# Kernel tuning notes

Measured on AMD Instinct MI355X. Metric: run time of the kernel, lower is better.

## Reference

```python
import jax, jax.numpy as jnp
import numpy as np

NUM_GRAPHS = 64


def gcn_conv(x, W, b, src, dst, deg_inv_sqrt, n_nodes):
    # x: [N, Fin] -> [N, Fout]; src/dst include self-loops
    h = x @ W                                   # [N, Fout]
    norm = deg_inv_sqrt[src] * deg_inv_sqrt[dst]  # [E+N]
    msg = h[src] * norm[:, None]                # gather + scale
    out = jax.ops.segment_sum(msg, dst, num_segments=n_nodes)  # scatter-add
    return out + b


def setup_inputs() -> dict:
    key = jax.random.key(0)
    ks = jax.random.split(key, 12)
    N, E, IND, H, OUT = 100000, 1600000, 128, 64, 2
    x = jax.random.normal(ks[0], (N, IND), dtype=jnp.float32)
    edge_index = jax.random.randint(ks[1], (2, E), 0, N, dtype=jnp.int64)
    batch = jnp.sort(jax.random.randint(ks[2], (N,), 0, NUM_GRAPHS, dtype=jnp.int64))
    def glorot(k, shape):
        lim = (6.0 / (shape[0] + shape[1])) ** 0.5
        return jax.random.uniform(k, shape, jnp.float32, -lim, lim)
    W1 = glorot(ks[3], (IND, 84)); b1 = jnp.zeros((84,), jnp.float32)
    W2 = glorot(ks[4], (84, H));   b2 = jnp.zeros((H,), jnp.float32)
    W3 = glorot(ks[5], (H, 32));   b3 = jnp.zeros((32,), jnp.float32)
    Wl = glorot(ks[6], (32, OUT)); bl = jnp.zeros((OUT,), jnp.float32)
    return {"x": x, "edge_index": edge_index, "batch": batch,
            "W1": W1, "b1": b1, "W2": W2, "b2": b2,
            "W3": W3, "b3": b3, "Wl": Wl, "bl": bl}


def reference(x, edge_index, batch, W1, b1, W2, b2, W3, b3, Wl, bl):
    n = x.shape[0]
    loops = jnp.arange(n, dtype=edge_index.dtype)
    # GCNConv adds self-loops before symmetric normalization
    src = jnp.concatenate([edge_index[0], loops])
    dst = jnp.concatenate([edge_index[1], loops])
    deg = jax.ops.segment_sum(jnp.ones_like(dst, dtype=x.dtype), dst, num_segments=n)
    dis = jnp.where(deg > 0, jax.lax.rsqrt(jnp.maximum(deg, 1.0)), 0.0)

    h = jax.nn.relu(gcn_conv(x, W1, b1, src, dst, dis, n))
    h = jax.nn.relu(gcn_conv(h, W2, b2, src, dst, dis, n))
    h = jax.nn.relu(gcn_conv(h, W3, b3, src, dst, dis, n))

    # global mean pool over graphs
    sums = jax.ops.segment_sum(h, batch, num_segments=NUM_GRAPHS)      # [G, 32]
    cnts = jax.ops.segment_sum(jnp.ones((n,), h.dtype), batch, num_segments=NUM_GRAPHS)
    pooled = sums / jnp.maximum(cnts, 1.0)[:, None]
    # dropout is identity in eval mode
    return pooled @ Wl + bl
```

## Files before the change

### kernel.cpp

```cpp
#include <hip/hip_runtime.h>
#include <hip/hip_bf16.h>

typedef __attribute__((ext_vector_type(8))) short bf16x8;
typedef __attribute__((ext_vector_type(4))) float f32x4;

__device__ inline short f2bf(float f) {
    __hip_bfloat16 h = __float2bfloat16(f);
    return *reinterpret_cast<short*>(&h);
}


__global__ void zero_k(float* __restrict__ p, int n) {
    for (int i = blockIdx.x * blockDim.x + threadIdx.x; i < n;
         i += gridDim.x * blockDim.x)
        p[i] = 0.0f;
}


__global__ __launch_bounds__(256) void bucket_hist_k(
    const int* __restrict__ dst, int* __restrict__ T, int E, int NB)
{
    __shared__ int hist[512];
    for (int b = threadIdx.x; b < NB; b += 256) hist[b] = 0;
    __syncthreads();
    int per = (E + gridDim.x - 1) / gridDim.x;
    int s = blockIdx.x * per;
    int e = min(E, s + per);
    for (int i = s + threadIdx.x; i < e; i += 256)
        atomicAdd(&hist[dst[i] >> 8], 1);
    __syncthreads();
    for (int b = threadIdx.x; b < NB; b += 256)
        T[b * gridDim.x + blockIdx.x] = hist[b];
}

__global__ __launch_bounds__(256) void scan_block_k(
    const int* __restrict__ in, int* __restrict__ out,
    int* __restrict__ bsum, int n)
{
    __shared__ int ts[256];
    int base = blockIdx.x * 2048;
    int i0 = base + threadIdx.x * 8;
    int vals[8];
    int s = 0;
#pragma unroll
    for (int j = 0; j < 8; ++j) {
        int v = (i0 + j) < n ? in[i0 + j] : 0;
        vals[j] = v; s += v;
    }
    ts[threadIdx.x] = s;
    __syncthreads();
    for (int d = 1; d < 256; d <<= 1) {
        int t = (threadIdx.x >= (unsigned)d) ? ts[threadIdx.x - d] : 0;
        __syncthreads();
        ts[threadIdx.x] += t;
        __syncthreads();
    }
    int run = ts[threadIdx.x] - s;
    if (threadIdx.x == 255) bsum[blockIdx.x] = ts[255];
#pragma unroll
    for (int j = 0; j < 8; ++j) {
        if (i0 + j < n) out[i0 + j] = run;
        run += vals[j];
    }
}

__global__ void scan_partials_k(int* __restrict__ bsum, int nb) {
    if (threadIdx.x == 0 && blockIdx.x == 0) {
        int run = 0;
        for (int i = 0; i < nb; ++i) { int t = bsum[i]; bsum[i] = run; run += t; }
    }
}

__global__ void scan_add_k(int* __restrict__ rp, const int* __restrict__ bsum,
                           int n, int E)
{
    int i = blockIdx.x * blockDim.x + threadIdx.x;
    if (i < n) rp[i] += bsum[i >> 11];
    if (i == 0) rp[n] = E;
}

__global__ __launch_bounds__(256) void bucket_scatter_k(
    const int* __restrict__ src, const int* __restrict__ dst,
    const int* __restrict__ Tsc, unsigned* __restrict__ pairs, int E, int NB)
{
    __shared__ int cur[512];
    for (int b = threadIdx.x; b < NB; b += 256)
        cur[b] = Tsc[b * gridDim.x + blockIdx.x];
    __syncthreads();
    int per = (E + gridDim.x - 1) / gridDim.x;
    int s = blockIdx.x * per;
    int e = min(E, s + per);
    for (int i = s + threadIdx.x; i < e; i += 256) {
        int d = dst[i];
        int pos = atomicAdd(&cur[d >> 8], 1);
        pairs[pos] = ((unsigned)(d & 255) << 24) | (unsigned)src[i];
    }
}

__global__ __launch_bounds__(256) void bucket_csr_k(
    const unsigned* __restrict__ pairs, const int* __restrict__ Tsc,
    int* __restrict__ row_ptr, float* __restrict__ dis,
    int* __restrict__ csr, int N, int E, int NB, int G)
{
    __shared__ int cnt[256];
    __shared__ int ts[256];
    __shared__ int cur[256];
    const int b = blockIdx.x;
    const int node0 = b << 8;
    const int e0 = Tsc[b * G];
    const int e1 = Tsc[(b + 1) * G];
    const int j = threadIdx.x;
    cnt[j] = 0;
    __syncthreads();
    for (int i = e0 + j; i < e1; i += 256)
        atomicAdd(&cnt[pairs[i] >> 24], 1);
    __syncthreads();
    int c = cnt[j];
    ts[j] = c;
    __syncthreads();
    for (int d = 1; d < 256; d <<= 1) {
        int t = (j >= d) ? ts[j - d] : 0;
        __syncthreads();
        ts[j] += t;
        __syncthreads();
    }
    int excl = ts[j] - c;
    int node = node0 + j;
    if (node < N) {
        row_ptr[node] = e0 + excl;
        dis[node] = rsqrtf(1.0f + (float)c);
    }
    cur[j] = e0 + excl;
    if (b == NB - 1 && j == 0) row_ptr[N] = E;
    __syncthreads();
    for (int i = e0 + j; i < e1; i += 256) {
        unsigned p = pairs[i];
        int pos = atomicAdd(&cur[p >> 24], 1);
        csr[pos] = (int)(p & 0xFFFFFFu);
    }
}


template<int FIN, int FOUT, int NKK, int CT>
__global__ void wfrag_build_k(const float* __restrict__ W,
                              __hip_bfloat16* __restrict__ out)
{
    int idx = blockIdx.x * 256 + threadIdx.x;
    if (idx >= CT * NKK * 64 * 8) return;
    int e = idx & 7;
    int lane = (idx >> 3) & 63;
    int t = idx >> 9;
    int kk = t % NKK, nn = t / NKK;
    int col = nn * 16 + (lane & 15);
    int k = kk * 32 + (lane >> 4) * 8 + e;
    float v = (k < FIN && col < FOUT) ? W[k * FOUT + col] : 0.f;
    out[idx] = __float2bfloat16(v);
}


template<int FIN>
__device__ inline bf16x8 load_a8f(const float* __restrict__ p, int k0) {
    bf16x8 r;
    if (k0 + 8 <= FIN) {
        float4 v0 = *reinterpret_cast<const float4*>(p + k0);
        float4 v1 = *reinterpret_cast<const float4*>(p + k0 + 4);
        r[0] = f2bf(v0.x); r[1] = f2bf(v0.y); r[2] = f2bf(v0.z); r[3] = f2bf(v0.w);
        r[4] = f2bf(v1.x); r[5] = f2bf(v1.y); r[6] = f2bf(v1.z); r[7] = f2bf(v1.w);
    } else {
#pragma unroll
        for (int e = 0; e < 8; ++e)
            r[e] = (k0 + e < FIN) ? f2bf(p[k0 + e]) : (short)0;
    }
    return r;
}

template<int FIN>
__device__ inline bf16x8 load_a8b(const __hip_bfloat16* __restrict__ p, int k0) {
    if (k0 + 8 <= FIN)
        return *reinterpret_cast<const bf16x8*>(p + k0);
    bf16x8 r;
    const short* ps = (const short*)p;
#pragma unroll
    for (int e = 0; e < 8; ++e)
        r[e] = (k0 + e < FIN) ? ps[k0 + e] : (short)0;
    return r;
}

template<typename TIN, int FIN, int SIN, int FOUT, int HS, int NKK, int CT>
__global__ __launch_bounds__(256) void gemm_mfma_v6(
    const TIN* __restrict__ in, const __hip_bfloat16* __restrict__ wfrag,
    const float* __restrict__ dis, __hip_bfloat16* __restrict__ hh, int n)
{
    const int tid = threadIdx.x;
    const long long base = (long long)blockIdx.x * 64;
    const int cnt = (int)min((long long)64, (long long)n - base);
    const int wv = tid >> 6, lane = tid & 63;
    const int rlo = lane & 15, kg = lane >> 4, kb = kg * 8;
    const int arow = wv * 16 + rlo;
    const long long row = base + arow;

    bf16x8 a[NKK];
    if (arow < cnt) {
        const TIN* p = &in[(size_t)row * SIN];
#pragma unroll
        for (int kk = 0; kk < NKK; ++kk) {
            if constexpr (sizeof(TIN) == 4)
                a[kk] = load_a8f<FIN>((const float*)p, kk * 32 + kb);
            else
                a[kk] = load_a8b<FIN>((const __hip_bfloat16*)p, kk * 32 + kb);
        }
    } else {
#pragma unroll
        for (int kk = 0; kk < NKK; ++kk)
            a[kk] = (bf16x8){0, 0, 0, 0, 0, 0, 0, 0};
    }

    f32x4 acc[CT];
#pragma unroll
    for (int nn = 0; nn < CT; ++nn) acc[nn] = (f32x4){0.f, 0.f, 0.f, 0.f};

#pragma unroll
    for (int nn = 0; nn < CT; ++nn) {
#pragma unroll
        for (int kk = 0; kk < NKK; ++kk) {
            bf16x8 b = *reinterpret_cast<const bf16x8*>(
                &wfrag[(size_t)((nn * NKK + kk) * 64 + lane) * 8]);
            acc[nn] = __builtin_amdgcn_mfma_f32_16x16x32_bf16(a[kk], b, acc[nn], 0, 0, 0);
        }
    }

    const int r0 = wv * 16 + kg * 4;
    float dv[4];
#pragma unroll
    for (int i = 0; i < 4; ++i)
        dv[i] = (r0 + i < cnt) ? dis[base + r0 + i] : 0.f;
#pragma unroll
    for (int nn = 0; nn < CT; ++nn) {
        const int col = nn * 16 + rlo;
        if (col < FOUT) {
#pragma unroll
            for (int i = 0; i < 4; ++i) {
                int r = r0 + i;
                if (r < cnt) {
                    __hip_bfloat16 o = __float2bfloat16(acc[nn][i] * dv[i]);
                    hh[(size_t)(base + r) * HS + col] = o;
                }
            }
        }
    }
}


template<int F, int HS, int SO, typename TOUT>
__global__ __launch_bounds__(256) void aggregate_v5(
    const __hip_bfloat16* __restrict__ hh, const int* __restrict__ row_ptr,
    const int* __restrict__ csr, const float* __restrict__ dis,
    const float* __restrict__ b, TOUT* __restrict__ out, int n)
{
    constexpr int FG = F / 4;
    long long idx = (long long)blockIdx.x * 256 + threadIdx.x;
    if (idx >= (long long)n * FG) return;
    int node = (int)(idx / FG);
    int fg = (int)(idx - (long long)node * FG);
    const int bf = fg * 4;

    const unsigned short* hs = (const unsigned short*)hh;
    auto lo16 = [](unsigned u) { return __uint_as_float(u << 16); };
    auto hi16 = [](unsigned u) { return __uint_as_float(u & 0xFFFF0000u); };

    uint2 su = *reinterpret_cast<const uint2*>(&hs[(size_t)node * HS + bf]);
    float a0 = lo16(su.x), a1 = hi16(su.x), a2 = lo16(su.y), a3 = hi16(su.y);
    float c0 = 0.f, c1 = 0.f, c2 = 0.f, c3 = 0.f;

    int e = row_ptr[node];
    const int e1 = row_ptr[node + 1];
    for (; e + 8 <= e1; e += 8) {
        int s0 = csr[e],     s1 = csr[e + 1], s2 = csr[e + 2], s3 = csr[e + 3];
        int s4 = csr[e + 4], s5 = csr[e + 5], s6 = csr[e + 6], s7 = csr[e + 7];
        uint2 u0 = *reinterpret_cast<const uint2*>(&hs[(size_t)s0 * HS + bf]);
        uint2 u1 = *reinterpret_cast<const uint2*>(&hs[(size_t)s1 * HS + bf]);
        uint2 u2 = *reinterpret_cast<const uint2*>(&hs[(size_t)s2 * HS + bf]);
        uint2 u3 = *reinterpret_cast<const uint2*>(&hs[(size_t)s3 * HS + bf]);
        uint2 u4 = *reinterpret_cast<const uint2*>(&hs[(size_t)s4 * HS + bf]);
        uint2 u5 = *reinterpret_cast<const uint2*>(&hs[(size_t)s5 * HS + bf]);
        uint2 u6 = *reinterpret_cast<const uint2*>(&hs[(size_t)s6 * HS + bf]);
        uint2 u7 = *reinterpret_cast<const uint2*>(&hs[(size_t)s7 * HS + bf]);
        a0 += lo16(u0.x); a1 += hi16(u0.x); a2 += lo16(u0.y); a3 += hi16(u0.y);
        c0 += lo16(u1.x); c1 += hi16(u1.x); c2 += lo16(u1.y); c3 += hi16(u1.y);
        a0 += lo16(u2.x); a1 += hi16(u2.x); a2 += lo16(u2.y); a3 += hi16(u2.y);
        c0 += lo16(u3.x); c1 += hi16(u3.x); c2 += lo16(u3.y); c3 += hi16(u3.y);
        a0 += lo16(u4.x); a1 += hi16(u4.x); a2 += lo16(u4.y); a3 += hi16(u4.y);
        c0 += lo16(u5.x); c1 += hi16(u5.x); c2 += lo16(u5.y); c3 += hi16(u5.y);
        a0 += lo16(u6.x); a1 += hi16(u6.x); a2 += lo16(u6.y); a3 += hi16(u6.y);
        c0 += lo16(u7.x); c1 += hi16(u7.x); c2 += lo16(u7.y); c3 += hi16(u7.y);
    }
    if (e + 4 <= e1) {
        int s0 = csr[e], s1 = csr[e + 1], s2 = csr[e + 2], s3 = csr[e + 3];
        uint2 u0 = *reinterpret_cast<const uint2*>(&hs[(size_t)s0 * HS + bf]);
        uint2 u1 = *reinterpret_cast<const uint2*>(&hs[(size_t)s1 * HS + bf]);
        uint2 u2 = *reinterpret_cast<const uint2*>(&hs[(size_t)s2 * HS + bf]);
        uint2 u3 = *reinterpret_cast<const uint2*>(&hs[(size_t)s3 * HS + bf]);
        a0 += lo16(u0.x); a1 += hi16(u0.x); a2 += lo16(u0.y); a3 += hi16(u0.y);
        c0 += lo16(u1.x); c1 += hi16(u1.x); c2 += lo16(u1.y); c3 += hi16(u1.y);
        a0 += lo16(u2.x); a1 += hi16(u2.x); a2 += lo16(u2.y); a3 += hi16(u2.y);
        c0 += lo16(u3.x); c1 += hi16(u3.x); c2 += lo16(u3.y); c3 += hi16(u3.y);
        e += 4;
    }
    for (; e < e1; ++e) {
        int s = csr[e];
        uint2 u = *reinterpret_cast<const uint2*>(&hs[(size_t)s * HS + bf]);
        a0 += lo16(u.x); a1 += hi16(u.x); a2 += lo16(u.y); a3 += hi16(u.y);
    }
    a0 += c0; a1 += c1; a2 += c2; a3 += c3;

    float d = dis[node];
    float4 bb = *reinterpret_cast<const float4*>(&b[bf]);
    float r0 = fmaxf(fmaf(d, a0, bb.x), 0.0f);
    float r1 = fmaxf(fmaf(d, a1, bb.y), 0.0f);
    float r2 = fmaxf(fmaf(d, a2, bb.z), 0.0f);
    float r3 = fmaxf(fmaf(d, a3, bb.w), 0.0f);

    if constexpr (sizeof(TOUT) == 2) {
        alignas(8) __hip_bfloat16 o[4];
        o[0] = __float2bfloat16(r0);
        o[1] = __float2bfloat16(r1);
        o[2] = __float2bfloat16(r2);
        o[3] = __float2bfloat16(r3);
        *reinterpret_cast<uint2*>(&((__hip_bfloat16*)out)[(size_t)node * SO + bf]) =
            *reinterpret_cast<const uint2*>(o);
    } else {
        float4 o;
        o.x = r0; o.y = r1; o.z = r2; o.w = r3;
        *reinterpret_cast<float4*>(&((float*)out)[(size_t)node * SO + bf]) = o;
    }
}


__global__ __launch_bounds__(256) void pool2_k(
    const float* __restrict__ h, const int* __restrict__ batch,
    float* __restrict__ sums, float* __restrict__ cnt, int n)
{
    constexpr int CHUNK = 1024;
    __shared__ float s[64 * 32];
    __shared__ float sc[64];
    for (int i = threadIdx.x; i < 64 * 32; i += 256) s[i] = 0.0f;
    if (threadIdx.x < 64) sc[threadIdx.x] = 0.0f;
    __syncthreads();

    long long start = (long long)blockIdx.x * CHUNK;
    long long end = start + CHUNK < n ? start + CHUNK : n;
    int total = (int)(end - start) * 32;
    for (int i = threadIdx.x; i < total; i += 256) {
        int r = i >> 5;
        int f = i & 31;
        int node = (int)start + r;
        int g = batch[node];
        atomicAdd(&s[g * 32 + f], h[(size_t)node * 32 + f]);
        if (f == 0) atomicAdd(&sc[g], 1.0f);
    }
    __syncthreads();
    for (int i = threadIdx.x; i < 64 * 32; i += 256) {
        float v = s[i];
        if (v != 0.0f) atomicAdd(&sums[i], v);
    }
    if (threadIdx.x < 64) {
        float v = sc[threadIdx.x];
        if (v != 0.0f) atomicAdd(&cnt[threadIdx.x], v);
    }
}

__global__ void head_k(const float* __restrict__ sums, const float* __restrict__ cnt,
                       const float* __restrict__ Wl, const float* __restrict__ bl,
                       float* __restrict__ out)
{
    int tid = threadIdx.x;
    if (tid < 128) {
        int g = tid >> 1;
        int o = tid & 1;
        float c = fmaxf(cnt[g], 1.0f);
        float a = 0.0f;
#pragma unroll
        for (int f = 0; f < 32; ++f)
            a += (sums[g * 32 + f] / c) * Wl[f * 2 + o];
        out[tid] = a + bl[o];
    }
}


extern "C" void kernel_launch(void* const* d_in, const int* in_sizes, int n_in,
                              void* d_out, int out_size, void* d_ws, size_t ws_size,
                              hipStream_t stream)
{
    const float* x   = (const float*)d_in[0];
    const int*   ei  = (const int*)d_in[1];
    const int*   bat = (const int*)d_in[2];
    const float* W1  = (const float*)d_in[3];
    const float* b1  = (const float*)d_in[4];
    const float* W2  = (const float*)d_in[5];
    const float* b2  = (const float*)d_in[6];
    const float* W3  = (const float*)d_in[7];
    const float* b3  = (const float*)d_in[8];
    const float* Wl  = (const float*)d_in[9];
    const float* bl  = (const float*)d_in[10];

    const int N = in_sizes[0] / 128;
    const int E = in_sizes[1] / 2;
    const int* src = ei;
    const int* dst = ei + E;

    const int NB = (N + 255) >> 8;
    const int G  = 128;
    const int NBG = NB * G;

    char* ws = (char*)d_ws;
    size_t off = 0;
    auto alloc = [&](size_t bytes) -> char* {
        char* p = ws + off;
        off += (bytes + 255) & ~(size_t)255;
        return p;
    };
    float* dis     = (float*)alloc((size_t)N * 4);
    int*   row_ptr = (int*)  alloc((size_t)(N + 1) * 4);
    int*   bsum    = (int*)  alloc(256 * 4);
    int*   csr     = (int*)  alloc((size_t)E * 4);
    int*   T       = (int*)  alloc((size_t)NBG * 4);
    int*   Tsc     = (int*)  alloc((size_t)(NBG + 1) * 4);
    __hip_bfloat16* WF1 = (__hip_bfloat16*)alloc(6 * 4 * 512 * 2);
    __hip_bfloat16* WF2 = (__hip_bfloat16*)alloc(4 * 3 * 512 * 2);
    __hip_bfloat16* WF3 = (__hip_bfloat16*)alloc(2 * 2 * 512 * 2);
    __hip_bfloat16* A = (__hip_bfloat16*)alloc((size_t)N * 96 * 2);
    __hip_bfloat16* B = (__hip_bfloat16*)alloc((size_t)N * 96 * 2);
    __hip_bfloat16* C = (__hip_bfloat16*)alloc((size_t)N * 64 * 2);
    float* D       = (float*)alloc((size_t)(64 * 32 + 64) * 4);
    unsigned* pairs = (unsigned*)C;

    dim3 blk(256);
    auto cdiv = [](long long a, long long b) { return (int)((a + b - 1) / b); };

    wfrag_build_k<128, 84, 4, 6><<<cdiv(6 * 4 * 512, 256), blk, 0, stream>>>(W1, WF1);
    wfrag_build_k< 84, 64, 3, 4><<<cdiv(4 * 3 * 512, 256), blk, 0, stream>>>(W2, WF2);
    wfrag_build_k< 64, 32, 2, 2><<<cdiv(2 * 2 * 512, 256), blk, 0, stream>>>(W3, WF3);

    bucket_hist_k<<<G, blk, 0, stream>>>(dst, T, E, NB);
    int nb_scan = cdiv(NBG, 2048);
    scan_block_k<<<nb_scan, blk, 0, stream>>>(T, Tsc, bsum, NBG);
    scan_partials_k<<<1, 64, 0, stream>>>(bsum, nb_scan);
    scan_add_k<<<cdiv(NBG, 256), blk, 0, stream>>>(Tsc, bsum, NBG, E);
    bucket_scatter_k<<<G, blk, 0, stream>>>(src, dst, Tsc, pairs, E, NB);
    bucket_csr_k<<<NB, blk, 0, stream>>>(pairs, Tsc, row_ptr, dis, csr, N, E, NB, G);

    gemm_mfma_v6<float, 128, 128, 84, 96, 4, 6><<<cdiv(N, 64), blk, 0, stream>>>(x, WF1, dis, A, N);
    aggregate_v5<84, 96, 96, __hip_bfloat16><<<cdiv((long long)N * 21, 256), blk, 0, stream>>>(
        A, row_ptr, csr, dis, b1, B, N);

    gemm_mfma_v6<__hip_bfloat16, 84, 96, 64, 64, 3, 4><<<cdiv(N, 64), blk, 0, stream>>>(B, WF2, dis, A, N);
    aggregate_v5<64, 64, 64, __hip_bfloat16><<<cdiv((long long)N * 16, 256), blk, 0, stream>>>(
        A, row_ptr, csr, dis, b2, C, N);

    gemm_mfma_v6<__hip_bfloat16, 64, 64, 32, 32, 2, 2><<<cdiv(N, 64), blk, 0, stream>>>(C, WF3, dis, A, N);
    aggregate_v5<32, 32, 32, float><<<cdiv((long long)N * 8, 256), blk, 0, stream>>>(
        A, row_ptr, csr, dis, b3, (float*)B, N);

    zero_k<<<cdiv(64 * 32 + 64, 256), blk, 0, stream>>>(D, 64 * 32 + 64);
    pool2_k<<<cdiv(N, 1024), blk, 0, stream>>>((float*)B, bat, D, D + 64 * 32, N);
    head_k<<<1, 128, 0, stream>>>(D, D + 64 * 32, Wl, bl, (float*)d_out);
}
```

Measured before the change: 288.8 us.

## Fuse final aggregation with mean pooling and merge weight-fragment kernels

The last GCN aggregation now pools directly: each thread aggregates its node's 4 features, applies bias and ReLU, and accumulates into shared-memory per-graph sums. This removes the fp32 intermediate write and read and one kernel launch. The three weight-fragment build kernels are merged into one launch, and the zeroing kernel is replaced by a memset. The cost is more shared-memory atomics per block, now spread across 256 node-features rather than chunked by 1024 nodes, and many more global atomic flushes because there are more blocks.

```diff
diff --git a/kernel.cpp b/kernel.cpp
--- a/kernel.cpp
+++ b/kernel.cpp
@@ -7,13 +7,6 @@
 __device__ inline short f2bf(float f) {
     __hip_bfloat16 h = __float2bfloat16(f);
     return *reinterpret_cast<short*>(&h);
-}
-
-
-__global__ void zero_k(float* __restrict__ p, int n) {
-    for (int i = blockIdx.x * blockDim.x + threadIdx.x; i < n;
-         i += gridDim.x * blockDim.x)
-        p[i] = 0.0f;
 }
 
 
@@ -141,12 +134,10 @@
 }
 
 
-template<int FIN, int FOUT, int NKK, int CT>
-__global__ void wfrag_build_k(const float* __restrict__ W,
-                              __hip_bfloat16* __restrict__ out)
-{
-    int idx = blockIdx.x * 256 + threadIdx.x;
-    if (idx >= CT * NKK * 64 * 8) return;
+__device__ inline void wfrag_seg(const float* __restrict__ W,
+                                 __hip_bfloat16* __restrict__ out, int idx,
+                                 int FIN, int FOUT, int NKK)
+{
     int e = idx & 7;
     int lane = (idx >> 3) & 63;
     int t = idx >> 9;
@@ -155,6 +146,17 @@
     int k = kk * 32 + (lane >> 4) * 8 + e;
     float v = (k < FIN && col < FOUT) ? W[k * FOUT + col] : 0.f;
     out[idx] = __float2bfloat16(v);
+}
+
+__global__ void wfrag_all_k(const float* __restrict__ W1,
+                            const float* __restrict__ W2,
+                            const float* __restrict__ W3,
+                            __hip_bfloat16* __restrict__ WF)
+{
+    int idx = blockIdx.x * 256 + threadIdx.x;
+    if (idx < 12288)       wfrag_seg(W1, WF,          idx,          128, 84, 4);
+    else if (idx < 18432)  wfrag_seg(W2, WF + 12288,  idx - 12288,   84, 64, 3);
+    else if (idx < 20480)  wfrag_seg(W3, WF + 18432,  idx - 18432,   64, 32, 2);
 }
 
 
@@ -336,27 +338,87 @@
 }
 
 
-__global__ __launch_bounds__(256) void pool2_k(
-    const float* __restrict__ h, const int* __restrict__ batch,
+__global__ __launch_bounds__(256) void agg_pool_k(
+    const __hip_bfloat16* __restrict__ hh, const int* __restrict__ row_ptr,
+    const int* __restrict__ csr, const float* __restrict__ dis,
+    const float* __restrict__ b, const int* __restrict__ batch,
     float* __restrict__ sums, float* __restrict__ cnt, int n)
 {
-    constexpr int CHUNK = 1024;
     __shared__ float s[64 * 32];
     __shared__ float sc[64];
     for (int i = threadIdx.x; i < 64 * 32; i += 256) s[i] = 0.0f;
     if (threadIdx.x < 64) sc[threadIdx.x] = 0.0f;
     __syncthreads();
 
-    long long start = (long long)blockIdx.x * CHUNK;
-    long long end = start + CHUNK < n ? start + CHUNK : n;
-    int total = (int)(end - start) * 32;
-    for (int i = threadIdx.x; i < total; i += 256) {
-        int r = i >> 5;
-        int f = i & 31;
-        int node = (int)start + r;
+    constexpr int HS = 32;
+    long long idx = (long long)blockIdx.x * 256 + threadIdx.x;
+    if (idx < (long long)n * 8) {
+        int node = (int)(idx >> 3);
+        int fg = (int)(idx & 7);
+        const int bf = fg * 4;
+
+        const unsigned short* hs = (const unsigned short*)hh;
+        auto lo16 = [](unsigned u) { return __uint_as_float(u << 16); };
+        auto hi16 = [](unsigned u) { return __uint_as_float(u & 0xFFFF0000u); };
+
+        uint2 su = *reinterpret_cast<const uint2*>(&hs[(size_t)node * HS + bf]);
+        float a0 = lo16(su.x), a1 = hi16(su.x), a2 = lo16(su.y), a3 = hi16(su.y);
+        float c0 = 0.f, c1 = 0.f, c2 = 0.f, c3 = 0.f;
+
+        int e = row_ptr[node];
+        const int e1 = row_ptr[node + 1];
+        for (; e + 8 <= e1; e += 8) {
+            int s0 = csr[e],     s1 = csr[e + 1], s2 = csr[e + 2], s3 = csr[e + 3];
+            int s4 = csr[e + 4], s5 = csr[e + 5], s6 = csr[e + 6], s7 = csr[e + 7];
+            uint2 u0 = *reinterpret_cast<const uint2*>(&hs[(size_t)s0 * HS + bf]);
+            uint2 u1 = *reinterpret_cast<const uint2*>(&hs[(size_t)s1 * HS + bf]);
+            uint2 u2 = *reinterpret_cast<const uint2*>(&hs[(size_t)s2 * HS + bf]);
+            uint2 u3 = *reinterpret_cast<const uint2*>(&hs[(size_t)s3 * HS + bf]);
+            uint2 u4 = *reinterpret_cast<const uint2*>(&hs[(size_t)s4 * HS + bf]);
+            uint2 u5 = *reinterpret_cast<const uint2*>(&hs[(size_t)s5 * HS + bf]);
+            uint2 u6 = *reinterpret_cast<const uint2*>(&hs[(size_t)s6 * HS + bf]);
+            uint2 u7 = *reinterpret_cast<const uint2*>(&hs[(size_t)s7 * HS + bf]);
+            a0 += lo16(u0.x); a1 += hi16(u0.x); a2 += lo16(u0.y); a3 += hi16(u0.y);
+            c0 += lo16(u1.x); c1 += hi16(u1.x); c2 += lo16(u1.y); c3 += hi16(u1.y);
+            a0 += lo16(u2.x); a1 += hi16(u2.x); a2 += lo16(u2.y); a3 += hi16(u2.y);
+            c0 += lo16(u3.x); c1 += hi16(u3.x); c2 += lo16(u3.y); c3 += hi16(u3.y);
+            a0 += lo16(u4.x); a1 += hi16(u4.x); a2 += lo16(u4.y); a3 += hi16(u4.y);
+            c0 += lo16(u5.x); c1 += hi16(u5.x); c2 += lo16(u5.y); c3 += hi16(u5.y);
+            a0 += lo16(u6.x); a1 += hi16(u6.x); a2 += lo16(u6.y); a3 += hi16(u6.y);
+            c0 += lo16(u7.x); c1 += hi16(u7.x); c2 += lo16(u7.y); c3 += hi16(u7.y);
+        }
+        if (e + 4 <= e1) {
+            int s0 = csr[e], s1 = csr[e + 1], s2 = csr[e + 2], s3 = csr[e + 3];
+            uint2 u0 = *reinterpret_cast<const uint2*>(&hs[(size_t)s0 * HS + bf]);
+            uint2 u1 = *reinterpret_cast<const uint2*>(&hs[(size_t)s1 * HS + bf]);
+            uint2 u2 = *reinterpret_cast<const uint2*>(&hs[(size_t)s2 * HS + bf]);
+            uint2 u3 = *reinterpret_cast<const uint2*>(&hs[(size_t)s3 * HS + bf]);
+            a0 += lo16(u0.x); a1 += hi16(u0.x); a2 += lo16(u0.y); a3 += hi16(u0.y);
+            c0 += lo16(u1.x); c1 += hi16(u1.x); c2 += lo16(u1.y); c3 += hi16(u1.y);
+            a0 += lo16(u2.x); a1 += hi16(u2.x); a2 += lo16(u2.y); a3 += hi16(u2.y);
+            c0 += lo16(u3.x); c1 += hi16(u3.x); c2 += lo16(u3.y); c3 += hi16(u3.y);
+            e += 4;
+        }
+        for (; e < e1; ++e) {
+            int sx = csr[e];
+            uint2 u = *reinterpret_cast<const uint2*>(&hs[(size_t)sx * HS + bf]);
+            a0 += lo16(u.x); a1 += hi16(u.x); a2 += lo16(u.y); a3 += hi16(u.y);
+        }
+        a0 += c0; a1 += c1; a2 += c2; a3 += c3;
+
+        float d = dis[node];
+        float4 bb = *reinterpret_cast<const float4*>(&b[bf]);
+        float r0 = fmaxf(fmaf(d, a0, bb.x), 0.0f);
+        float r1 = fmaxf(fmaf(d, a1, bb.y), 0.0f);
+        float r2 = fmaxf(fmaf(d, a2, bb.z), 0.0f);
+        float r3 = fmaxf(fmaf(d, a3, bb.w), 0.0f);
+
         int g = batch[node];
-        atomicAdd(&s[g * 32 + f], h[(size_t)node * 32 + f]);
-        if (f == 0) atomicAdd(&sc[g], 1.0f);
+        atomicAdd(&s[g * 32 + bf + 0], r0);
+        atomicAdd(&s[g * 32 + bf + 1], r1);
+        atomicAdd(&s[g * 32 + bf + 2], r2);
+        atomicAdd(&s[g * 32 + bf + 3], r3);
+        if (fg == 0) atomicAdd(&sc[g], 1.0f);
     }
     __syncthreads();
     for (int i = threadIdx.x; i < 64 * 32; i += 256) {
@@ -425,21 +487,21 @@
     int*   csr     = (int*)  alloc((size_t)E * 4);
     int*   T       = (int*)  alloc((size_t)NBG * 4);
     int*   Tsc     = (int*)  alloc((size_t)(NBG + 1) * 4);
-    __hip_bfloat16* WF1 = (__hip_bfloat16*)alloc(6 * 4 * 512 * 2);
-    __hip_bfloat16* WF2 = (__hip_bfloat16*)alloc(4 * 3 * 512 * 2);
-    __hip_bfloat16* WF3 = (__hip_bfloat16*)alloc(2 * 2 * 512 * 2);
+    __hip_bfloat16* WF = (__hip_bfloat16*)alloc(20480 * 2);
     __hip_bfloat16* A = (__hip_bfloat16*)alloc((size_t)N * 96 * 2);
     __hip_bfloat16* B = (__hip_bfloat16*)alloc((size_t)N * 96 * 2);
     __hip_bfloat16* C = (__hip_bfloat16*)alloc((size_t)N * 64 * 2);
     float* D       = (float*)alloc((size_t)(64 * 32 + 64) * 4);
     unsigned* pairs = (unsigned*)C;
+    __hip_bfloat16* WF2 = WF + 12288;
+    __hip_bfloat16* WF3 = WF + 18432;
 
     dim3 blk(256);
     auto cdiv = [](long long a, long long b) { return (int)((a + b - 1) / b); };
 
-    wfrag_build_k<128, 84, 4, 6><<<cdiv(6 * 4 * 512, 256), blk, 0, stream>>>(W1, WF1);
-    wfrag_build_k< 84, 64, 3, 4><<<cdiv(4 * 3 * 512, 256), blk, 0, stream>>>(W2, WF2);
-    wfrag_build_k< 64, 32, 2, 2><<<cdiv(2 * 2 * 512, 256), blk, 0, stream>>>(W3, WF3);
+    hipMemsetAsync(D, 0, (64 * 32 + 64) * 4, stream);
+
+    wfrag_all_k<<<cdiv(20480, 256), blk, 0, stream>>>(W1, W2, W3, WF);
 
     bucket_hist_k<<<G, blk, 0, stream>>>(dst, T, E, NB);
     int nb_scan = cdiv(NBG, 2048);
@@ -449,7 +511,7 @@
     bucket_scatter_k<<<G, blk, 0, stream>>>(src, dst, Tsc, pairs, E, NB);
     bucket_csr_k<<<NB, blk, 0, stream>>>(pairs, Tsc, row_ptr, dis, csr, N, E, NB, G);
 
-    gemm_mfma_v6<float, 128, 128, 84, 96, 4, 6><<<cdiv(N, 64), blk, 0, stream>>>(x, WF1, dis, A, N);
+    gemm_mfma_v6<float, 128, 128, 84, 96, 4, 6><<<cdiv(N, 64), blk, 0, stream>>>(x, WF, dis, A, N);
     aggregate_v5<84, 96, 96, __hip_bfloat16><<<cdiv((long long)N * 21, 256), blk, 0, stream>>>(
         A, row_ptr, csr, dis, b1, B, N);
 
@@ -458,10 +520,8 @@
         A, row_ptr, csr, dis, b2, C, N);
 
     gemm_mfma_v6<__hip_bfloat16, 64, 64, 32, 32, 2, 2><<<cdiv(N, 64), blk, 0, stream>>>(C, WF3, dis, A, N);
-    aggregate_v5<32, 32, 32, float><<<cdiv((long long)N * 8, 256), blk, 0, stream>>>(
-        A, row_ptr, csr, dis, b3, (float*)B, N);
-
-    zero_k<<<cdiv(64 * 32 + 64, 256), blk, 0, stream>>>(D, 64 * 32 + 64);
-    pool2_k<<<cdiv(N, 1024), blk, 0, stream>>>((float*)B, bat, D, D + 64 * 32, N);
+    agg_pool_k<<<cdiv((long long)N * 8, 256), blk, 0, stream>>>(
+        A, row_ptr, csr, dis, b3, bat, D, D + 64 * 32, N);
+
     head_k<<<1, 128, 0, stream>>>(D, D + 64 * 32, Wl, bl, (float*)d_out);
 }
```

After: 268.0 us. 1.08x faster.
